# Optimization experiments

Measured on AMD Instinct MI355X. Metric: run time of the kernel, lower is better.

The kernel has to match this reference:

```python
import jax, jax.numpy as jnp
import numpy as np

N_NODES = 100000
N_EDGES = 1600000
D_IN = 128
D_OUT = 32
DROP_P = 0.6
NEG_SLOPE = 0.2


def setup_inputs() -> dict:
    key = jax.random.key(0)
    ks = jax.random.split(key, 10)
    x = jax.random.normal(ks[0], (N_NODES, D_IN), dtype=jnp.float32)
    edge_index = jax.random.randint(ks[1], (2, N_EDGES), 0, N_NODES, dtype=jnp.int32)
    drop_u = jax.random.uniform(ks[2], (N_NODES, D_IN), dtype=jnp.float32)
    s = 1.0 / np.sqrt(D_IN)
    W_src = jax.random.normal(ks[3], (D_IN, D_OUT), dtype=jnp.float32) * s
    W_dst = jax.random.normal(ks[4], (D_IN, D_OUT), dtype=jnp.float32) * s
    att_src = jax.random.normal(ks[5], (D_OUT,), dtype=jnp.float32) * s
    att_dst = jax.random.normal(ks[6], (D_OUT,), dtype=jnp.float32) * s
    bias_gat = jax.random.normal(ks[7], (D_OUT,), dtype=jnp.float32) * 0.01
    W_lin = jax.random.normal(ks[8], (D_OUT, D_OUT), dtype=jnp.float32) / np.sqrt(D_OUT)
    b_lin = jax.random.normal(ks[9], (D_OUT,), dtype=jnp.float32) * 0.01
    return {"x": x, "edge_index": edge_index, "drop_u": drop_u,
            "W_src": W_src, "W_dst": W_dst, "att_src": att_src,
            "att_dst": att_dst, "bias_gat": bias_gat,
            "W_lin": W_lin, "b_lin": b_lin}


def reference(x, edge_index, drop_u, W_src, W_dst, att_src, att_dst,
              bias_gat, W_lin, b_lin):
    n = x.shape[0]
    # F.dropout(x, p=0.6, training=True) with deterministic uniform draws
    keep = (drop_u > DROP_P).astype(x.dtype)
    xd = x * keep / (1.0 - DROP_P)

    # GATConv (heads=1): separate src/dst linear maps
    h_src = xd @ W_src                      # [N, D_OUT]
    h_dst = xd @ W_dst                      # [N, D_OUT]
    a_src = h_src @ att_src                 # [N]
    a_dst = h_dst @ att_dst                 # [N]

    # add_self_loops=True (PyG default)
    loops = jnp.arange(n, dtype=edge_index.dtype)
    src = jnp.concatenate([edge_index[0], loops])   # [E+N]
    dst = jnp.concatenate([edge_index[1], loops])   # [E+N]

    e = a_src[src] + a_dst[dst]                      # per-edge raw score
    e = jnp.where(e > 0, e, NEG_SLOPE * e)           # leaky_relu(0.2)

    # segment softmax over destination-node neighborhoods
    e_max = jax.ops.segment_max(e, dst, num_segments=n)  # every node has a self loop
    e_exp = jnp.exp(e - e_max[dst])
    denom = jax.ops.segment_sum(e_exp, dst, num_segments=n)
    alpha = e_exp / denom[dst]                       # [E+N]

    # scatter-add aggregation of weighted source features
    msg = h_src[src] * alpha[:, None]                # [E+N, D_OUT]
    out = jax.ops.segment_sum(msg, dst, num_segments=n) + bias_gat

    # residual linear + relu + log_softmax
    out = out + out @ W_lin + b_lin
    out = jax.nn.relu(out)
    logp = jax.nn.log_softmax(out, axis=1)
    return logp, alpha
```

## Files before the change

kernel.cpp:

```cpp
#include <hip/hip_runtime.h>
#include <hip/hip_bf16.h>
#include <math.h>

#define D_IN   128
#define D_OUT  32
#define NEG_SLOPE 0.2f
#define DROP_P 0.6f
#define KEEP_SCALE 2.5f

#define NPB     128
#define NB      782
#define CAPB    2816
#define CHUNK   4096
#define BT      512
#define EPT     8
#define SRC_BITS 17
#define SRC_MASK ((1u << SRC_BITS) - 1)

#define SLICES  4
#define NPS     32
#define CAPS    896
#define EPT3    11

typedef __attribute__((ext_vector_type(8))) short fragAB;
typedef __attribute__((ext_vector_type(4))) float fragCD;

__device__ __forceinline__ void atomicMaxF(float* addr, float v) {
    if (v >= 0.0f) atomicMax((int*)addr, __float_as_int(v));
    else           atomicMin((unsigned int*)addr, __float_as_uint(v));
}

__device__ __forceinline__ unsigned pack_bf16(float lo, float hi) {
    __hip_bfloat16 l = __float2bfloat16(lo);
    __hip_bfloat16 h = __float2bfloat16(hi);
    unsigned short lb, hb;
    __builtin_memcpy(&lb, &l, 2);
    __builtin_memcpy(&hb, &h, 2);
    return (unsigned)lb | ((unsigned)hb << 16);
}

__device__ __forceinline__ unsigned short f2bf(float f) {
    __hip_bfloat16 h = __float2bfloat16(f);
    unsigned short u;
    __builtin_memcpy(&u, &h, 2);
    return u;
}

__global__ void k_fold(const float* __restrict__ W_src, const float* __restrict__ W_dst,
                       const float* __restrict__ att_src, const float* __restrict__ att_dst,
                       float* __restrict__ v_src, float* __restrict__ v_dst,
                       int* __restrict__ gcur, uint4* __restrict__ wfrag) {
    int gi = blockIdx.x * blockDim.x + threadIdx.x;
    if (gi < NB) gcur[gi] = gi * CAPB;
    if (gi < 512) {
        int tile = gi >> 8;
        int kb   = (gi >> 6) & 3;
        int lane = gi & 63;
        int grp = lane >> 4, col = lane & 15;
        int kbase = kb * 32 + grp * 8;
        int cidx  = tile * 16 + col;
        unsigned o0 = pack_bf16(W_src[(kbase + 0) * D_OUT + cidx], W_src[(kbase + 1) * D_OUT + cidx]);
        unsigned o1 = pack_bf16(W_src[(kbase + 2) * D_OUT + cidx], W_src[(kbase + 3) * D_OUT + cidx]);
        unsigned o2 = pack_bf16(W_src[(kbase + 4) * D_OUT + cidx], W_src[(kbase + 5) * D_OUT + cidx]);
        unsigned o3 = pack_bf16(W_src[(kbase + 6) * D_OUT + cidx], W_src[(kbase + 7) * D_OUT + cidx]);
        wfrag[gi] = make_uint4(o0, o1, o2, o3);
    }
    if (blockIdx.x == 0) {
        int k = threadIdx.x;
        if (k < D_IN) {
            float s = 0.f, d = 0.f;
            #pragma unroll
            for (int c = 0; c < D_OUT; ++c) {
                s += W_src[k * D_OUT + c] * att_src[c];
                d += W_dst[k * D_OUT + c] * att_dst[c];
            }
            v_src[k] = s;
            v_dst[k] = d;
        }
    }
}

__global__ __launch_bounds__(256) void k_nodes_mfma(
    const float* __restrict__ x, const float* __restrict__ drop_u,
    const uint4* __restrict__ wfrag,
    const float* __restrict__ v_src, const float* __restrict__ v_dst,
    unsigned short* __restrict__ h_bf16,
    float* __restrict__ a_src, float* __restrict__ a_dst,
    int n)
{
    int tid  = threadIdx.x;
    int wv   = tid >> 6;
    int lane = tid & 63;
    int nbase = blockIdx.x * 64 + wv * 16;
    int row = lane & 15, grp = lane >> 4;

    int arow_raw = nbase + row;
    bool aact = arow_raw < n;
    int arow = aact ? arow_raw : (n - 1);
    const float* xr = x      + (size_t)arow * D_IN;
    const float* dr = drop_u + (size_t)arow * D_IN;

    fragCD c0 = {0.f, 0.f, 0.f, 0.f};
    fragCD c1 = {0.f, 0.f, 0.f, 0.f};
    float ps = 0.f, pd = 0.f;

    #pragma unroll
    for (int kb = 0; kb < 4; ++kb) {
        int k0 = kb * 32 + grp * 8;
        float4 xa = *(const float4*)(xr + k0);
        float4 xb = *(const float4*)(xr + k0 + 4);
        float4 da = *(const float4*)(dr + k0);
        float4 db = *(const float4*)(dr + k0 + 4);
        float f0 = da.x > DROP_P ? xa.x * KEEP_SCALE : 0.f;
        float f1 = da.y > DROP_P ? xa.y * KEEP_SCALE : 0.f;
        float f2 = da.z > DROP_P ? xa.z * KEEP_SCALE : 0.f;
        float f3 = da.w > DROP_P ? xa.w * KEEP_SCALE : 0.f;
        float f4 = db.x > DROP_P ? xb.x * KEEP_SCALE : 0.f;
        float f5 = db.y > DROP_P ? xb.y * KEEP_SCALE : 0.f;
        float f6 = db.z > DROP_P ? xb.z * KEEP_SCALE : 0.f;
        float f7 = db.w > DROP_P ? xb.w * KEEP_SCALE : 0.f;

        float4 vs1 = *(const float4*)(v_src + k0);
        float4 vs2 = *(const float4*)(v_src + k0 + 4);
        float4 vd1 = *(const float4*)(v_dst + k0);
        float4 vd2 = *(const float4*)(v_dst + k0 + 4);
        ps += f0 * vs1.x + f1 * vs1.y + f2 * vs1.z + f3 * vs1.w
            + f4 * vs2.x + f5 * vs2.y + f6 * vs2.z + f7 * vs2.w;
        pd += f0 * vd1.x + f1 * vd1.y + f2 * vd1.z + f3 * vd1.w
            + f4 * vd2.x + f5 * vd2.y + f6 * vd2.z + f7 * vd2.w;

        union { unsigned u[4]; fragAB v; } af;
        af.u[0] = pack_bf16(f0, f1);
        af.u[1] = pack_bf16(f2, f3);
        af.u[2] = pack_bf16(f4, f5);
        af.u[3] = pack_bf16(f6, f7);

        fragAB b0 = *reinterpret_cast<const fragAB*>(&wfrag[kb * 64 + lane]);
        fragAB b1 = *reinterpret_cast<const fragAB*>(&wfrag[256 + kb * 64 + lane]);
        c0 = __builtin_amdgcn_mfma_f32_16x16x32_bf16(af.v, b0, c0, 0, 0, 0);
        c1 = __builtin_amdgcn_mfma_f32_16x16x32_bf16(af.v, b1, c1, 0, 0, 0);
    }

    ps += __shfl_xor(ps, 16); ps += __shfl_xor(ps, 32);
    pd += __shfl_xor(pd, 16); pd += __shfl_xor(pd, 32);
    if (grp == 0 && aact) { a_src[arow_raw] = ps; a_dst[arow_raw] = pd; }

    #pragma unroll
    for (int r = 0; r < 4; ++r) {
        int onode = nbase + grp * 4 + r;
        if (onode < n) {
            h_bf16[(size_t)onode * D_OUT + row]      = f2bf(c0[r]);
            h_bf16[(size_t)onode * D_OUT + 16 + row] = f2bf(c1[r]);
        }
    }
}

__global__ __launch_bounds__(256) void k_nodes(
    const float* __restrict__ x, const float* __restrict__ drop_u,
    const float* __restrict__ W_src,
    const float* __restrict__ v_src, const float* __restrict__ v_dst,
    float* __restrict__ h_src, float* __restrict__ a_src, float* __restrict__ a_dst,
    float* __restrict__ e_max, float* __restrict__ denom,
    float* __restrict__ agg, int n, int init_aux)
{
    int gt = blockIdx.x * 256 + threadIdx.x;
    int node_raw = gt >> 2;
    int sub = gt & 3;
    bool act = node_raw < n;
    int node = act ? node_raw : (n - 1);

    const float4* xr4 = (const float4*)(x      + (size_t)node * D_IN) + sub * 8;
    const float4* dr4 = (const float4*)(drop_u + (size_t)node * D_IN) + sub * 8;
    const float*  wb  = W_src + sub * 32 * D_OUT;
    const float4* vsp = (const float4*)v_src + sub * 8;
    const float4* vdp = (const float4*)v_dst + sub * 8;

    float4 xv[8];
    #pragma unroll
    for (int q = 0; q < 8; ++q) {
        float4 xl = xr4[q];
        float4 dl = dr4[q];
        xv[q].x = dl.x > DROP_P ? xl.x * KEEP_SCALE : 0.f;
        xv[q].y = dl.y > DROP_P ? xl.y * KEEP_SCALE : 0.f;
        xv[q].z = dl.z > DROP_P ? xl.z * KEEP_SCALE : 0.f;
        xv[q].w = dl.w > DROP_P ? xl.w * KEEP_SCALE : 0.f;
    }

    float acc[D_OUT];
    #pragma unroll
    for (int c = 0; c < D_OUT; ++c) acc[c] = 0.f;
    float ps = 0.f, pd = 0.f;

    #pragma unroll
    for (int q = 0; q < 8; ++q) {
        float4 vs4 = vsp[q];
        float4 vd4 = vdp[q];
        ps += xv[q].x * vs4.x + xv[q].y * vs4.y + xv[q].z * vs4.z + xv[q].w * vs4.w;
        pd += xv[q].x * vd4.x + xv[q].y * vd4.y + xv[q].z * vd4.z + xv[q].w * vd4.w;
        #pragma unroll
        for (int kk = 0; kk < 4; ++kk) {
            float xk = (kk == 0) ? xv[q].x : (kk == 1) ? xv[q].y : (kk == 2) ? xv[q].z : xv[q].w;
            const float4* wrow = (const float4*)(wb + (q * 4 + kk) * D_OUT);
            #pragma unroll
            for (int c4 = 0; c4 < 8; ++c4) {
                float4 w = wrow[c4];
                acc[c4 * 4 + 0] += xk * w.x;
                acc[c4 * 4 + 1] += xk * w.y;
                acc[c4 * 4 + 2] += xk * w.z;
                acc[c4 * 4 + 3] += xk * w.w;
            }
        }
    }

    #pragma unroll
    for (int c = 0; c < D_OUT; ++c) {
        acc[c] += __shfl_xor(acc[c], 1);
        acc[c] += __shfl_xor(acc[c], 2);
    }
    ps += __shfl_xor(ps, 1); ps += __shfl_xor(ps, 2);
    pd += __shfl_xor(pd, 1); pd += __shfl_xor(pd, 2);

    if (act) {
        if (sub == 0) {
            a_src[node] = ps;
            a_dst[node] = pd;
            if (init_aux) { e_max[node] = -3.0e38f; denom[node] = 0.f; }
        }
        float o[8];
        if (sub == 0) {
            #pragma unroll
            for (int i = 0; i < 8; ++i) o[i] = acc[i];
        } else if (sub == 1) {
            #pragma unroll
            for (int i = 0; i < 8; ++i) o[i] = acc[8 + i];
        } else if (sub == 2) {
            #pragma unroll
            for (int i = 0; i < 8; ++i) o[i] = acc[16 + i];
        } else {
            #pragma unroll
            for (int i = 0; i < 8; ++i) o[i] = acc[24 + i];
        }
        float4* hb = (float4*)(h_src + (size_t)node * D_OUT + sub * 8);
        hb[0] = make_float4(o[0], o[1], o[2], o[3]);
        hb[1] = make_float4(o[4], o[5], o[6], o[7]);
        if (init_aux) {
            float4* ab = (float4*)(agg + (size_t)node * D_OUT + sub * 8);
            ab[0] = make_float4(0.f, 0.f, 0.f, 0.f);
            ab[1] = make_float4(0.f, 0.f, 0.f, 0.f);
        }
    }
}

__global__ __launch_bounds__(BT) void k_binsort(
    const int* __restrict__ ei, int E, int n,
    int* __restrict__ gcur, unsigned* __restrict__ binned)
{
    __shared__ int A[1024], B[1024];
    __shared__ int excl[NB + 1];
    __shared__ int lcur[NB];
    __shared__ int gpos[NB];
    __shared__ unsigned stage[CHUNK];
    __shared__ unsigned short sbk[CHUNK];

    int tid = threadIdx.x;
    int T   = E + n;
    int base = blockIdx.x * CHUNK;

    for (int k = tid; k < 1024; k += BT) A[k] = 0;
    __syncthreads();

    unsigned rec[EPT];
    int      bk [EPT];
    #pragma unroll
    for (int e = 0; e < EPT; ++e) {
        int i = base + e * BT + tid;
        if (i < T) {
            int s, d;
            if (i < E) { s = ei[i]; d = ei[E + i]; }
            else       { s = d = i - E; }
            int b    = d >> 7;
            int drel = d & 127;
            rec[e] = (unsigned)s | ((unsigned)drel << SRC_BITS);
            bk[e]  = b;
            atomicAdd(&A[b], 1);
        } else bk[e] = -1;
    }
    __syncthreads();

    int* cur = A; int* nxt = B;
    for (int off = 1; off < 1024; off <<= 1) {
        for (int k = tid; k < 1024; k += BT) {
            int v = cur[k];
            if (k >= off) v += cur[k - off];
            nxt[k] = v;
        }
        __syncthreads();
        int* t = cur; cur = nxt; nxt = t;
    }

    for (int b = tid; b < NB; b += BT) {
        int e0 = b ? cur[b - 1] : 0;
        excl[b] = e0;
        lcur[b] = e0;
        int c = cur[b] - e0;
        gpos[b] = c ? atomicAdd(&gcur[b], c) : 0;
    }
    if (tid == 0) excl[NB] = cur[NB - 1];
    __syncthreads();

    #pragma unroll
    for (int e = 0; e < EPT; ++e) {
        if (bk[e] >= 0) {
            int slot = atomicAdd(&lcur[bk[e]], 1);
            stage[slot] = rec[e];
            sbk[slot]   = (unsigned short)bk[e];
        }
    }
    __syncthreads();

    int tot = excl[NB];
    for (int j = tid; j < tot; j += BT) {
        int b = sbk[j];
        unsigned gd = (unsigned)(gpos[b] + (j - excl[b]));
        if (gd < (unsigned)(b + 1) * CAPB)
            binned[gd] = stage[j];
    }
}

__global__ __launch_bounds__(256) void k_bucket3(
    const unsigned* __restrict__ binned, const int* __restrict__ gcur,
    const float* __restrict__ a_src, const float* __restrict__ a_dst,
    const unsigned short* __restrict__ h_bf16,
    const float* __restrict__ bias_gat, const float* __restrict__ W_lin,
    const float* __restrict__ b_lin,
    float* __restrict__ inv_out,
    float* __restrict__ io, int n)
{
    __shared__ unsigned grp_e[CAPS];
    __shared__ float    ex[CAPS];
    __shared__ int A[NPS];
    __shared__ int ends[NPS];
    __shared__ int ncur[NPS];
    __shared__ float Wl[D_OUT * D_OUT];
    __shared__ float ul[8][D_OUT];

    int tid   = threadIdx.x;
    int lin   = (blockIdx.x & 7) * ((NB * SLICES) >> 3) + (blockIdx.x >> 3);
    int b     = lin >> 2;
    int slice = lin & 3;
    int n0    = b * NPB + slice * NPS;
    int nn    = n - n0; if (nn > NPS) nn = NPS;
    if (nn <= 0) return;

    for (int i = tid; i < D_OUT * D_OUT; i += 256) Wl[i] = W_lin[i];
    if (tid < NPS) A[tid] = 0;
    __syncthreads();

    int cnt = gcur[b] - b * CAPB;
    if (cnt > CAPB) cnt = CAPB;
    const unsigned* src = binned + (size_t)b * CAPB;

    unsigned rr[EPT3];
    #pragma unroll
    for (int e = 0; e < EPT3; ++e) {
        int j = tid + e * 256;
        if (j < cnt) {
            unsigned r = src[j];
            rr[e] = r;
            int drel = r >> SRC_BITS;
            if ((drel >> 5) == slice) atomicAdd(&A[drel & 31], 1);
        }
    }
    __syncthreads();

    if (tid < NPS) {
        int v = A[tid];
        #pragma unroll
        for (int off = 1; off < NPS; off <<= 1) {
            int u = __shfl_up(v, off, NPS);
            if (tid >= off) v += u;
        }
        ends[tid] = v;
        ncur[tid] = v - A[tid];
    }
    __syncthreads();

    #pragma unroll
    for (int e = 0; e < EPT3; ++e) {
        int j = tid + e * 256;
        if (j < cnt) {
            unsigned r = rr[e];
            int drel = r >> SRC_BITS;
            if ((drel >> 5) == slice) {
                int pos = atomicAdd(&ncur[drel & 31], 1);
                if (pos < CAPS) grp_e[pos] = r;
            }
        }
    }
    __syncthreads();

    int g = tid >> 5, lane = tid & 31;
    float bg = bias_gat[lane];
    float bl = b_lin[lane];

    for (int nr = g; nr < nn; nr += 8) {
        int st = nr ? ends[nr - 1] : 0;
        int en = ends[nr];
        if (st > CAPS) st = CAPS;
        if (en > CAPS) en = CAPS;
        int node = n0 + nr;
        float adst = a_dst[node];

        float ss = 0.f;
        for (int j = st + lane; j < en; j += 32) {
            float e = a_src[grp_e[j] & SRC_MASK] + adst;
            e = e > 0.f ? e : NEG_SLOPE * e;
            float v = expf(e);
            ex[j] = v;
            ss += v;
        }
        #pragma unroll
        for (int o = 16; o; o >>= 1) ss += __shfl_xor(ss, o);
        float inv = 1.0f / ss;
        if (lane == 0) inv_out[node] = inv;

        float acc0 = 0.f, acc1 = 0.f, acc2 = 0.f, acc3 = 0.f;
        int j = st;
        for (; j + 3 < en; j += 4) {
            unsigned r0 = grp_e[j], r1 = grp_e[j + 1], r2 = grp_e[j + 2], r3 = grp_e[j + 3];
            float h0 = __uint_as_float((unsigned)h_bf16[((r0 & SRC_MASK) << 5) + lane] << 16);
            float h1 = __uint_as_float((unsigned)h_bf16[((r1 & SRC_MASK) << 5) + lane] << 16);
            float h2 = __uint_as_float((unsigned)h_bf16[((r2 & SRC_MASK) << 5) + lane] << 16);
            float h3 = __uint_as_float((unsigned)h_bf16[((r3 & SRC_MASK) << 5) + lane] << 16);
            acc0 += h0 * ex[j];
            acc1 += h1 * ex[j + 1];
            acc2 += h2 * ex[j + 2];
            acc3 += h3 * ex[j + 3];
        }
        for (; j < en; ++j)
            acc0 += __uint_as_float((unsigned)h_bf16[((grp_e[j] & SRC_MASK) << 5) + lane] << 16) * ex[j];

        float u = ((acc0 + acc1) + (acc2 + acc3)) * inv + bg;
        ul[g][lane] = u;
        float r2 = u + bl;
        #pragma unroll 8
        for (int k = 0; k < D_OUT; ++k)
            r2 += ul[g][k] * Wl[k * D_OUT + lane];
        r2 = fmaxf(r2, 0.f);

        float mm = r2;
        #pragma unroll
        for (int o = 16; o; o >>= 1) mm = fmaxf(mm, __shfl_xor(mm, o));
        float e2 = expf(r2 - mm);
        float s2 = e2;
        #pragma unroll
        for (int o = 16; o; o >>= 1) s2 += __shfl_xor(s2, o);
        io[(size_t)node * D_OUT + lane] = r2 - mm - logf(s2);
    }
}

__global__ void k_alpha(const int* __restrict__ ei, int E, int n,
                        const float* __restrict__ a_src, const float* __restrict__ a_dst,
                        const float* __restrict__ inv,
                        float* __restrict__ alpha_out)
{
    int i = blockIdx.x * blockDim.x + threadIdx.x;
    int T = E + n;
    if (i >= T) return;
    int s, d;
    if (i < E) { s = ei[i]; d = ei[E + i]; }
    else       { s = d = i - E; }
    float e = a_src[s] + a_dst[d];
    e = e > 0.f ? e : NEG_SLOPE * e;
    alpha_out[i] = expf(e) * inv[d];
}

__global__ void k_edge_score(const int* __restrict__ ei, int E, int n,
                             const float* __restrict__ a_src, const float* __restrict__ a_dst,
                             float* __restrict__ score_out, float* __restrict__ e_max)
{
    int total = E + n;
    int i = blockIdx.x * blockDim.x + threadIdx.x;
    if (i >= total) return;
    int s, d;
    if (i < E) { s = ei[i]; d = ei[E + i]; }
    else       { s = d = i - E; }
    float e = a_src[s] + a_dst[d];
    e = e > 0.f ? e : NEG_SLOPE * e;
    score_out[i] = e;
    atomicMaxF(&e_max[d], e);
}

__global__ void k_edge_exp(const int* __restrict__ ei, int E, int n,
                           const float* __restrict__ e_max,
                           float* __restrict__ score_io, float* __restrict__ denom)
{
    int total = E + n;
    int i = blockIdx.x * blockDim.x + threadIdx.x;
    if (i >= total) return;
    int d = (i < E) ? ei[E + i] : (i - E);
    float ex = expf(score_io[i] - e_max[d]);
    score_io[i] = ex;
    atomicAdd(&denom[d], ex);
}

__global__ __launch_bounds__(256) void k_edge_agg(
    const int* __restrict__ ei, int E, int n,
    const float* __restrict__ h_src, const float* __restrict__ denom,
    float* __restrict__ alpha_io, float* __restrict__ agg)
{
    int tid  = threadIdx.x;
    int loc  = tid >> 5;
    int lane = tid & 31;
    int i = blockIdx.x * 8 + loc;
    int total = E + n;
    if (i >= total) return;
    int s, d;
    if (i < E) { s = ei[i]; d = ei[E + i]; }
    else       { s = d = i - E; }
    float alpha = alpha_io[i] / denom[d];
    if (lane == 0) alpha_io[i] = alpha;
    float m = h_src[(size_t)s * D_OUT + lane] * alpha;
    atomicAdd(&agg[(size_t)d * D_OUT + lane], m);
}

__global__ __launch_bounds__(256) void k_final(
    const float* __restrict__ bias_gat, const float* __restrict__ W_lin,
    const float* __restrict__ b_lin, float* __restrict__ io, int n)
{
    __shared__ float Wl[D_OUT * D_OUT];
    __shared__ float ul[8][D_OUT];

    int tid = threadIdx.x;
    for (int i = tid; i < D_OUT * D_OUT; i += 256) Wl[i] = W_lin[i];
    __syncthreads();

    int loc  = tid >> 5;
    int lane = tid & 31;
    int node = blockIdx.x * 8 + loc;

    float u = 0.f;
    if (node < n) u = io[(size_t)node * D_OUT + lane] + bias_gat[lane];
    ul[loc][lane] = u;
    __syncthreads();

    float r = u + b_lin[lane];
    #pragma unroll 8
    for (int k = 0; k < D_OUT; ++k)
        r += ul[loc][k] * Wl[k * D_OUT + lane];
    r = fmaxf(r, 0.f);

    float m = r;
    #pragma unroll
    for (int off = 16; off; off >>= 1) m = fmaxf(m, __shfl_xor(m, off));
    float ex = expf(r - m);
    float ssum = ex;
    #pragma unroll
    for (int off = 16; off; off >>= 1) ssum += __shfl_xor(ssum, off);
    float logp = r - m - logf(ssum);

    if (node < n) io[(size_t)node * D_OUT + lane] = logp;
}

extern "C" void kernel_launch(void* const* d_in, const int* in_sizes, int n_in,
                              void* d_out, int out_size, void* d_ws, size_t ws_size,
                              hipStream_t stream)
{
    const float* x        = (const float*)d_in[0];
    const int*   ei       = (const int*)  d_in[1];
    const float* drop_u   = (const float*)d_in[2];
    const float* W_src    = (const float*)d_in[3];
    const float* W_dst    = (const float*)d_in[4];
    const float* att_src  = (const float*)d_in[5];
    const float* att_dst  = (const float*)d_in[6];
    const float* bias_gat = (const float*)d_in[7];
    const float* W_lin    = (const float*)d_in[8];
    const float* b_lin    = (const float*)d_in[9];

    const int N = in_sizes[0] / D_IN;
    const int E = in_sizes[1] / 2;
    const int total = E + N;

    float* ws = (float*)d_ws;

    float* v_src = ws;
    float* v_dst = ws + 128;
    float* h_src = ws + 256;
    unsigned short* h_bf16 = (unsigned short*)h_src;
    float* a_src = h_src + (size_t)N * D_OUT;
    float* a_dst = a_src + N;
    float* m_buf = a_dst + N;
    float* i_buf = m_buf + N;

    size_t idx = 256 + (size_t)N * D_OUT + 4 * (size_t)N;
    int* gcur = (int*)(ws + idx);       idx += NB + 2;
    idx = (idx + 3) & ~(size_t)3;
    uint4* wfrag = (uint4*)(ws + idx);  idx += 2048;
    unsigned* binned = (unsigned*)(ws + idx); idx += (size_t)NB * CAPB;
    size_t need_bytes = idx * sizeof(float);

    float* logp_out  = (float*)d_out;
    float* alpha_out = (float*)d_out + (size_t)N * D_OUT;

    int mfmaBlocks = (N + 63) / 64;
    int nodeBlocks = (int)(((size_t)N * 4 + 255) / 256);
    int nodeBlocks8 = (N + 7) / 8;
    int eb = (total + 255) / 256;

    bool fits = (ws_size >= need_bytes) && (N < (1 << SRC_BITS)) && (N <= NB * NPB);

    if (fits) {
        k_fold<<<7, 128, 0, stream>>>(W_src, W_dst, att_src, att_dst,
                                      v_src, v_dst, gcur, wfrag);
        k_nodes_mfma<<<mfmaBlocks, 256, 0, stream>>>(x, drop_u, wfrag, v_src, v_dst,
                                                     h_bf16, a_src, a_dst, N);
        int nchunk = (total + CHUNK - 1) / CHUNK;
        k_binsort<<<nchunk, BT, 0, stream>>>(ei, E, N, gcur, binned);
        k_bucket3<<<NB * SLICES, 256, 0, stream>>>(binned, gcur, a_src, a_dst, h_bf16,
                                                   bias_gat, W_lin, b_lin,
                                                   i_buf, logp_out, N);
        k_alpha<<<eb, 256, 0, stream>>>(ei, E, N, a_src, a_dst, i_buf, alpha_out);
    } else {
        k_fold<<<7, 128, 0, stream>>>(W_src, W_dst, att_src, att_dst,
                                      v_src, v_dst, gcur, wfrag);
        k_nodes<<<nodeBlocks, 256, 0, stream>>>(x, drop_u, W_src, v_src, v_dst,
                                                h_src, a_src, a_dst,
                                                m_buf, i_buf, logp_out, N, 1);
        k_edge_score<<<eb, 256, 0, stream>>>(ei, E, N, a_src, a_dst, alpha_out, m_buf);
        k_edge_exp<<<eb, 256, 0, stream>>>(ei, E, N, m_buf, alpha_out, i_buf);
        int aggBlocks = (total + 7) / 8;
        k_edge_agg<<<aggBlocks, 256, 0, stream>>>(ei, E, N, h_src, i_buf, alpha_out, logp_out);
        k_final<<<nodeBlocks8, 256, 0, stream>>>(bias_gat, W_lin, b_lin, logp_out, N);
    }
}
```

Measured before the change: 125.0 us.

## Use full 64-lane wavefronts per node in bucket aggregation kernel

The aggregation kernel moves from 256 to 512 threads per block and assigns one 64-lane wavefront per destination node instead of a 32-lane group. The two 32-lane halves split each node's edge list by parity, then combine their partial sums with a cross-half shuffle. The intent is to use all lanes of each wavefront on the gather, where before half of every 64-wide wave sat idle. The cost is larger blocks, which may lower occupancy, plus a reduction step and some half-idle epilogue work.

After: 141.6 us. 1.13x slower.

```diff
diff --git a/kernel.cpp b/kernel.cpp
--- a/kernel.cpp
+++ b/kernel.cpp
@@ -20,7 +20,8 @@
 #define SLICES  4
 #define NPS     32
 #define CAPS    896
-#define EPT3    11
+#define BT3     512
+#define EPT3B   6
 
 typedef __attribute__((ext_vector_type(8))) short fragAB;
 typedef __attribute__((ext_vector_type(4))) float fragCD;
@@ -327,7 +328,7 @@
     }
 }
 
-__global__ __launch_bounds__(256) void k_bucket3(
+__global__ __launch_bounds__(BT3) void k_bucket3(
     const unsigned* __restrict__ binned, const int* __restrict__ gcur,
     const float* __restrict__ a_src, const float* __restrict__ a_dst,
     const unsigned short* __restrict__ h_bf16,
@@ -352,7 +353,7 @@
     int nn    = n - n0; if (nn > NPS) nn = NPS;
     if (nn <= 0) return;
 
-    for (int i = tid; i < D_OUT * D_OUT; i += 256) Wl[i] = W_lin[i];
+    for (int i = tid; i < D_OUT * D_OUT; i += BT3) Wl[i] = W_lin[i];
     if (tid < NPS) A[tid] = 0;
     __syncthreads();
 
@@ -360,10 +361,10 @@
     if (cnt > CAPB) cnt = CAPB;
     const unsigned* src = binned + (size_t)b * CAPB;
 
-    unsigned rr[EPT3];
-    #pragma unroll
-    for (int e = 0; e < EPT3; ++e) {
-        int j = tid + e * 256;
+    unsigned rr[EPT3B];
+    #pragma unroll
+    for (int e = 0; e < EPT3B; ++e) {
+        int j = tid + e * BT3;
         if (j < cnt) {
             unsigned r = src[j];
             rr[e] = r;
@@ -386,8 +387,8 @@
     __syncthreads();
 
     #pragma unroll
-    for (int e = 0; e < EPT3; ++e) {
-        int j = tid + e * 256;
+    for (int e = 0; e < EPT3B; ++e) {
+        int j = tid + e * BT3;
         if (j < cnt) {
             unsigned r = rr[e];
             int drel = r >> SRC_BITS;
@@ -399,11 +400,14 @@
     }
     __syncthreads();
 
-    int g = tid >> 5, lane = tid & 31;
-    float bg = bias_gat[lane];
-    float bl = b_lin[lane];
-
-    for (int nr = g; nr < nn; nr += 8) {
+    int wv   = tid >> 6;
+    int lane = tid & 63;
+    int ch   = lane & 31;
+    int eo   = lane >> 5;
+    float bg = bias_gat[ch];
+    float bl = b_lin[ch];
+
+    for (int nr = wv; nr < nn; nr += 8) {
         int st = nr ? ends[nr - 1] : 0;
         int en = ends[nr];
         if (st > CAPS) st = CAPS;
@@ -412,7 +416,7 @@
         float adst = a_dst[node];
 
         float ss = 0.f;
-        for (int j = st + lane; j < en; j += 32) {
+        for (int j = st + lane; j < en; j += 64) {
             float e = a_src[grp_e[j] & SRC_MASK] + adst;
             e = e > 0.f ? e : NEG_SLOPE * e;
             float v = expf(e);
@@ -420,32 +424,36 @@
             ss += v;
         }
         #pragma unroll
-        for (int o = 16; o; o >>= 1) ss += __shfl_xor(ss, o);
+        for (int o = 32; o; o >>= 1) ss += __shfl_xor(ss, o);
         float inv = 1.0f / ss;
         if (lane == 0) inv_out[node] = inv;
 
         float acc0 = 0.f, acc1 = 0.f, acc2 = 0.f, acc3 = 0.f;
-        int j = st;
-        for (; j + 3 < en; j += 4) {
-            unsigned r0 = grp_e[j], r1 = grp_e[j + 1], r2 = grp_e[j + 2], r3 = grp_e[j + 3];
-            float h0 = __uint_as_float((unsigned)h_bf16[((r0 & SRC_MASK) << 5) + lane] << 16);
-            float h1 = __uint_as_float((unsigned)h_bf16[((r1 & SRC_MASK) << 5) + lane] << 16);
-            float h2 = __uint_as_float((unsigned)h_bf16[((r2 & SRC_MASK) << 5) + lane] << 16);
-            float h3 = __uint_as_float((unsigned)h_bf16[((r3 & SRC_MASK) << 5) + lane] << 16);
+        int j = st + eo;
+        for (; j + 6 < en; j += 8) {
+            unsigned r0 = grp_e[j],     r1 = grp_e[j + 2];
+            unsigned r2 = grp_e[j + 4], r3 = grp_e[j + 6];
+            float h0 = __uint_as_float((unsigned)h_bf16[((r0 & SRC_MASK) << 5) + ch] << 16);
+            float h1 = __uint_as_float((unsigned)h_bf16[((r1 & SRC_MASK) << 5) + ch] << 16);
+            float h2 = __uint_as_float((unsigned)h_bf16[((r2 & SRC_MASK) << 5) + ch] << 16);
+            float h3 = __uint_as_float((unsigned)h_bf16[((r3 & SRC_MASK) << 5) + ch] << 16);
             acc0 += h0 * ex[j];
-            acc1 += h1 * ex[j + 1];
-            acc2 += h2 * ex[j + 2];
-            acc3 += h3 * ex[j + 3];
-        }
-        for (; j < en; ++j)
-            acc0 += __uint_as_float((unsigned)h_bf16[((grp_e[j] & SRC_MASK) << 5) + lane] << 16) * ex[j];
-
-        float u = ((acc0 + acc1) + (acc2 + acc3)) * inv + bg;
-        ul[g][lane] = u;
+            acc1 += h1 * ex[j + 2];
+            acc2 += h2 * ex[j + 4];
+            acc3 += h3 * ex[j + 6];
+        }
+        for (; j < en; j += 2)
+            acc0 += __uint_as_float((unsigned)h_bf16[((grp_e[j] & SRC_MASK) << 5) + ch] << 16) * ex[j];
+
+        float acc = (acc0 + acc1) + (acc2 + acc3);
+        acc += __shfl_xor(acc, 32);
+
+        float u = acc * inv + bg;
+        if (eo == 0) ul[wv][ch] = u;
         float r2 = u + bl;
         #pragma unroll 8
         for (int k = 0; k < D_OUT; ++k)
-            r2 += ul[g][k] * Wl[k * D_OUT + lane];
+            r2 += ul[wv][k] * Wl[k * D_OUT + ch];
         r2 = fmaxf(r2, 0.f);
 
         float mm = r2;
@@ -455,7 +463,8 @@
         float s2 = e2;
         #pragma unroll
         for (int o = 16; o; o >>= 1) s2 += __shfl_xor(s2, o);
-        io[(size_t)node * D_OUT + lane] = r2 - mm - logf(s2);
+        if (eo == 0)
+            io[(size_t)node * D_OUT + ch] = r2 - mm - logf(s2);
     }
 }
 
@@ -616,7 +625,7 @@
                                                      h_bf16, a_src, a_dst, N);
         int nchunk = (total + CHUNK - 1) / CHUNK;
         k_binsort<<<nchunk, BT, 0, stream>>>(ei, E, N, gcur, binned);
-        k_bucket3<<<NB * SLICES, 256, 0, stream>>>(binned, gcur, a_src, a_dst, h_bf16,
+        k_bucket3<<<NB * SLICES, BT3, 0, stream>>>(binned, gcur, a_src, a_dst, h_bf16,
                                                    bias_gat, W_lin, b_lin,
                                                    i_buf, logp_out, N);
         k_alpha<<<eb, 256, 0, stream>>>(ei, E, N, a_src, a_dst, i_buf, alpha_out);
```

## Compute edge exp scores in binsort and carry them in binned records

Applied to the files above, without the earlier changes.

The binsort kernel now gathers a_src[s] and a_dst[d] for each edge, applies leaky-relu and exp, and stores the result beside the packed src/drel word as a uint2 record. The bucket kernel then reads precomputed exp values instead of doing a random a_src gather and exp per edge, and drops the separate ex shared array. The aggregation loop is also unrolled from 4 to 8 accumulators for more memory-level parallelism. In exchange the binned buffer and shared staging double in size, which adds global traffic and LDS pressure in binsort and may lower its occupancy.

Result: slower. 128.8 us (+3.1%).

```diff
diff --git a/kernel.cpp b/kernel.cpp
--- a/kernel.cpp
+++ b/kernel.cpp
@@ -253,13 +253,14 @@
 
 __global__ __launch_bounds__(BT) void k_binsort(
     const int* __restrict__ ei, int E, int n,
-    int* __restrict__ gcur, unsigned* __restrict__ binned)
+    const float* __restrict__ a_src, const float* __restrict__ a_dst,
+    int* __restrict__ gcur, uint2* __restrict__ binned)
 {
     __shared__ int A[1024], B[1024];
     __shared__ int excl[NB + 1];
     __shared__ int lcur[NB];
     __shared__ int gpos[NB];
-    __shared__ unsigned stage[CHUNK];
+    __shared__ uint2 stage[CHUNK];
     __shared__ unsigned short sbk[CHUNK];
 
     int tid = threadIdx.x;
@@ -269,8 +270,8 @@
     for (int k = tid; k < 1024; k += BT) A[k] = 0;
     __syncthreads();
 
-    unsigned rec[EPT];
-    int      bk [EPT];
+    uint2 rec[EPT];
+    int   bk [EPT];
     #pragma unroll
     for (int e = 0; e < EPT; ++e) {
         int i = base + e * BT + tid;
@@ -280,7 +281,10 @@
             else       { s = d = i - E; }
             int b    = d >> 7;
             int drel = d & 127;
-            rec[e] = (unsigned)s | ((unsigned)drel << SRC_BITS);
+            float sc = a_src[s] + a_dst[d];
+            sc = sc > 0.f ? sc : NEG_SLOPE * sc;
+            rec[e].x = (unsigned)s | ((unsigned)drel << SRC_BITS);
+            rec[e].y = __float_as_uint(expf(sc));
             bk[e]  = b;
             atomicAdd(&A[b], 1);
         } else bk[e] = -1;
@@ -328,16 +332,14 @@
 }
 
 __global__ __launch_bounds__(256) void k_bucket3(
-    const unsigned* __restrict__ binned, const int* __restrict__ gcur,
-    const float* __restrict__ a_src, const float* __restrict__ a_dst,
+    const uint2* __restrict__ binned, const int* __restrict__ gcur,
     const unsigned short* __restrict__ h_bf16,
     const float* __restrict__ bias_gat, const float* __restrict__ W_lin,
     const float* __restrict__ b_lin,
     float* __restrict__ inv_out,
     float* __restrict__ io, int n)
 {
-    __shared__ unsigned grp_e[CAPS];
-    __shared__ float    ex[CAPS];
+    __shared__ uint2 grp[CAPS];
     __shared__ int A[NPS];
     __shared__ int ends[NPS];
     __shared__ int ncur[NPS];
@@ -358,16 +360,16 @@
 
     int cnt = gcur[b] - b * CAPB;
     if (cnt > CAPB) cnt = CAPB;
-    const unsigned* src = binned + (size_t)b * CAPB;
-
-    unsigned rr[EPT3];
+    const uint2* src = binned + (size_t)b * CAPB;
+
+    uint2 rr[EPT3];
     #pragma unroll
     for (int e = 0; e < EPT3; ++e) {
         int j = tid + e * 256;
         if (j < cnt) {
-            unsigned r = src[j];
+            uint2 r = src[j];
             rr[e] = r;
-            int drel = r >> SRC_BITS;
+            int drel = r.x >> SRC_BITS;
             if ((drel >> 5) == slice) atomicAdd(&A[drel & 31], 1);
         }
     }
@@ -389,11 +391,11 @@
     for (int e = 0; e < EPT3; ++e) {
         int j = tid + e * 256;
         if (j < cnt) {
-            unsigned r = rr[e];
-            int drel = r >> SRC_BITS;
+            uint2 r = rr[e];
+            int drel = r.x >> SRC_BITS;
             if ((drel >> 5) == slice) {
                 int pos = atomicAdd(&ncur[drel & 31], 1);
-                if (pos < CAPS) grp_e[pos] = r;
+                if (pos < CAPS) grp[pos] = make_uint2(r.x & SRC_MASK, r.y);
             }
         }
     }
@@ -409,38 +411,47 @@
         if (st > CAPS) st = CAPS;
         if (en > CAPS) en = CAPS;
         int node = n0 + nr;
-        float adst = a_dst[node];
 
         float ss = 0.f;
-        for (int j = st + lane; j < en; j += 32) {
-            float e = a_src[grp_e[j] & SRC_MASK] + adst;
-            e = e > 0.f ? e : NEG_SLOPE * e;
-            float v = expf(e);
-            ex[j] = v;
-            ss += v;
-        }
+        for (int j = st + lane; j < en; j += 32)
+            ss += __uint_as_float(grp[j].y);
         #pragma unroll
         for (int o = 16; o; o >>= 1) ss += __shfl_xor(ss, o);
         float inv = 1.0f / ss;
         if (lane == 0) inv_out[node] = inv;
 
         float acc0 = 0.f, acc1 = 0.f, acc2 = 0.f, acc3 = 0.f;
+        float acc4 = 0.f, acc5 = 0.f, acc6 = 0.f, acc7 = 0.f;
         int j = st;
-        for (; j + 3 < en; j += 4) {
-            unsigned r0 = grp_e[j], r1 = grp_e[j + 1], r2 = grp_e[j + 2], r3 = grp_e[j + 3];
-            float h0 = __uint_as_float((unsigned)h_bf16[((r0 & SRC_MASK) << 5) + lane] << 16);
-            float h1 = __uint_as_float((unsigned)h_bf16[((r1 & SRC_MASK) << 5) + lane] << 16);
-            float h2 = __uint_as_float((unsigned)h_bf16[((r2 & SRC_MASK) << 5) + lane] << 16);
-            float h3 = __uint_as_float((unsigned)h_bf16[((r3 & SRC_MASK) << 5) + lane] << 16);
-            acc0 += h0 * ex[j];
-            acc1 += h1 * ex[j + 1];
-            acc2 += h2 * ex[j + 2];
-            acc3 += h3 * ex[j + 3];
-        }
-        for (; j < en; ++j)
-            acc0 += __uint_as_float((unsigned)h_bf16[((grp_e[j] & SRC_MASK) << 5) + lane] << 16) * ex[j];
-
-        float u = ((acc0 + acc1) + (acc2 + acc3)) * inv + bg;
+        for (; j + 7 < en; j += 8) {
+            uint2 p0 = grp[j],     p1 = grp[j + 1];
+            uint2 p2 = grp[j + 2], p3 = grp[j + 3];
+            uint2 p4 = grp[j + 4], p5 = grp[j + 5];
+            uint2 p6 = grp[j + 6], p7 = grp[j + 7];
+            float h0 = __uint_as_float((unsigned)h_bf16[(p0.x << 5) + lane] << 16);
+            float h1 = __uint_as_float((unsigned)h_bf16[(p1.x << 5) + lane] << 16);
+            float h2 = __uint_as_float((unsigned)h_bf16[(p2.x << 5) + lane] << 16);
+            float h3 = __uint_as_float((unsigned)h_bf16[(p3.x << 5) + lane] << 16);
+            float h4 = __uint_as_float((unsigned)h_bf16[(p4.x << 5) + lane] << 16);
+            float h5 = __uint_as_float((unsigned)h_bf16[(p5.x << 5) + lane] << 16);
+            float h6 = __uint_as_float((unsigned)h_bf16[(p6.x << 5) + lane] << 16);
+            float h7 = __uint_as_float((unsigned)h_bf16[(p7.x << 5) + lane] << 16);
+            acc0 += h0 * __uint_as_float(p0.y);
+            acc1 += h1 * __uint_as_float(p1.y);
+            acc2 += h2 * __uint_as_float(p2.y);
+            acc3 += h3 * __uint_as_float(p3.y);
+            acc4 += h4 * __uint_as_float(p4.y);
+            acc5 += h5 * __uint_as_float(p5.y);
+            acc6 += h6 * __uint_as_float(p6.y);
+            acc7 += h7 * __uint_as_float(p7.y);
+        }
+        for (; j < en; ++j) {
+            uint2 p = grp[j];
+            acc0 += __uint_as_float((unsigned)h_bf16[(p.x << 5) + lane] << 16)
+                  * __uint_as_float(p.y);
+        }
+
+        float u = (((acc0 + acc1) + (acc2 + acc3)) + ((acc4 + acc5) + (acc6 + acc7))) * inv + bg;
         ul[g][lane] = u;
         float r2 = u + bl;
         #pragma unroll 8
@@ -596,7 +607,7 @@
     int* gcur = (int*)(ws + idx);       idx += NB + 2;
     idx = (idx + 3) & ~(size_t)3;
     uint4* wfrag = (uint4*)(ws + idx);  idx += 2048;
-    unsigned* binned = (unsigned*)(ws + idx); idx += (size_t)NB * CAPB;
+    uint2* binned = (uint2*)(ws + idx); idx += 2 * (size_t)NB * CAPB;
     size_t need_bytes = idx * sizeof(float);
 
     float* logp_out  = (float*)d_out;
@@ -615,8 +626,8 @@
         k_nodes_mfma<<<mfmaBlocks, 256, 0, stream>>>(x, drop_u, wfrag, v_src, v_dst,
                                                      h_bf16, a_src, a_dst, N);
         int nchunk = (total + CHUNK - 1) / CHUNK;
-        k_binsort<<<nchunk, BT, 0, stream>>>(ei, E, N, gcur, binned);
-        k_bucket3<<<NB * SLICES, 256, 0, stream>>>(binned, gcur, a_src, a_dst, h_bf16,
+        k_binsort<<<nchunk, BT, 0, stream>>>(ei, E, N, a_src, a_dst, gcur, binned);
+        k_bucket3<<<NB * SLICES, 256, 0, stream>>>(binned, gcur, h_bf16,
                                                    bias_gat, W_lin, b_lin,
                                                    i_buf, logp_out, N);
         k_alpha<<<eb, 256, 0, stream>>>(ei, E, N, a_src, a_dst, i_buf, alpha_out);
```
